# Kernel tuning notes

Hardware: AMD Instinct MI355X
Metric: run time of the kernel (lower is better)

The kernel has to match this reference:

```python
import jax, jax.numpy as jnp
import numpy as np

B, S, HID = 2, 2048, 3584
NH, NKV, HD = 16, 8, 256
WINDOW = 1024
SOFTCAP = 50.0


def setup_inputs() -> dict:
    key = jax.random.key(0)
    ks = jax.random.split(key, 8)
    hidden_states = jax.random.normal(ks[0], (B, S, HID), dtype=jnp.float32)
    attention_mask = jnp.ones((B, S), dtype=bool)
    position_ids = jnp.tile(jnp.arange(S, dtype=jnp.int32), (B, 1))
    # rotary tables indexed by position, last dim = head_dim
    inv_freq = 1.0 / (10000.0 ** (jnp.arange(0, HD, 2, dtype=jnp.float32) / HD))
    t = jnp.arange(S, dtype=jnp.float32)
    freqs = jnp.outer(t, inv_freq)  # [S, HD/2]
    emb = jnp.concatenate([freqs, freqs], axis=-1)  # [S, HD]
    sin, cos = jnp.sin(emb), jnp.cos(emb)
    causal_mask = jnp.tril(jnp.ones((1, 1, S, S), dtype=bool))
    sc = 0.02
    Wq = jax.random.normal(ks[1], (HID, NH * HD), dtype=jnp.float32) * sc
    Wk = jax.random.normal(ks[2], (HID, NKV * HD), dtype=jnp.float32) * sc
    Wv = jax.random.normal(ks[3], (HID, NKV * HD), dtype=jnp.float32) * sc
    Wo = jax.random.normal(ks[4], (NH * HD, HID), dtype=jnp.float32) * sc
    return {"hidden_states": hidden_states, "attention_mask": attention_mask,
            "position_ids": position_ids, "sin": sin, "cos": cos,
            "causal_mask": causal_mask, "Wq": Wq, "Wk": Wk, "Wv": Wv, "Wo": Wo}


def _rotate_half(x):
    x1, x2 = x[..., : x.shape[-1] // 2], x[..., x.shape[-1] // 2 :]
    return jnp.concatenate((-x2, x1), axis=-1)


def reference(hidden_states, attention_mask, position_ids, sin, cos, causal_mask, Wq, Wk, Wv, Wo):
    b, s, _ = hidden_states.shape
    q = (hidden_states @ Wq).reshape(b, s, NH, HD)
    k = (hidden_states @ Wk).reshape(b, s, NKV, HD)
    v = (hidden_states @ Wv).reshape(b, s, NKV, HD)

    # RoPE, applied in [b, h, s, d] layout as in the original
    s_ = sin[position_ids][:, None, :, :]  # [b,1,s,d]
    c_ = cos[position_ids][:, None, :, :]
    qh = q.transpose(0, 2, 1, 3)
    kh = k.transpose(0, 2, 1, 3)
    qh = qh * c_ + _rotate_half(qh) * s_
    kh = kh * c_ + _rotate_half(kh) * s_
    q = qh.transpose(0, 2, 1, 3)  # [b,s,nh,d]
    k = kh.transpose(0, 2, 1, 3)  # [b,s,nkv,d]

    # GQA: repeat kv heads to match query heads
    groups = NH // NKV
    k = jnp.repeat(k, groups, axis=2)  # [b,s,nh,d]
    v = jnp.repeat(v, groups, axis=2)

    # combine causal + padding masks, then sliding-window (even layer)
    mask = causal_mask[:, :, :s, :s] & attention_mask[:, None, None, :]  # [b,1,s,s]
    mask = jnp.broadcast_to(mask, (b, 1, s, s))
    far_past = jnp.tril(jnp.ones((s, s), dtype=bool), k=-WINDOW)[None, None]
    mask = mask & ~far_past

    neg = jnp.finfo(jnp.float32).min
    bias = jnp.where(mask, 0.0, neg).astype(jnp.float32)

    scale = HD ** -0.5
    logits = jnp.einsum("bqhd,bkhd->bhqk", q, k) * scale
    # Gemma2 logit softcapping
    logits = SOFTCAP * jnp.tanh(logits / SOFTCAP)
    logits = logits + bias
    probs = jax.nn.softmax(logits, axis=-1)
    out = jnp.einsum("bhqk,bkhd->bqhd", probs, v)
    out = out.reshape(b, s, NH * HD)
    return out @ Wo
```

## Files before the change

### kernel.cpp

```cpp
#include <hip/hip_runtime.h>
#include <hip/hip_bf16.h>

typedef __bf16 bf16x8_t __attribute__((ext_vector_type(8)));
typedef __bf16 bf16x4_t __attribute__((ext_vector_type(4)));
typedef short s16x4_t  __attribute__((ext_vector_type(4)));
typedef float f32x4_t  __attribute__((ext_vector_type(4)));

#define NB 2
#define NS 2048
#define NHID 3584
#define NHEADS 16
#define NKVH 8
#define DH 256
#define WIN 1024

__device__ __forceinline__ float bf2f(ushort u) {
  union { unsigned v; float f; } x; x.v = ((unsigned)u) << 16; return x.f;
}
__device__ __forceinline__ ushort f2bf(float f) {
  unsigned x = __builtin_bit_cast(unsigned, f);
  unsigned r = (x + 0x7fffu + ((x >> 16) & 1u)) >> 16;
  return (ushort)r;
}

__device__ __forceinline__ void gload16(const void* g, void* l) {
  __builtin_amdgcn_global_load_lds((const __attribute__((address_space(1))) void*)g,
                                   (__attribute__((address_space(3))) void*)l, 16, 0, 0);
}

__device__ __forceinline__ f32x4_t mfma_pv(s16x4_t a, s16x4_t b, f32x4_t c) {
#if __has_builtin(__builtin_amdgcn_mfma_f32_16x16x16_bf16)
  return __builtin_amdgcn_mfma_f32_16x16x16_bf16(
      __builtin_bit_cast(bf16x4_t, a), __builtin_bit_cast(bf16x4_t, b), c, 0, 0, 0);
#else
  return __builtin_amdgcn_mfma_f32_16x16x16bf16_1k(a, b, c, 0, 0, 0);
#endif
}

__device__ __forceinline__ float pexp(float s) {
  float e = __expf(fminf(s * 0.0025f, 80.f));
  float th = __fdividef(e - 1.f, e + 1.f);
  return __expf(50.f * th);
}

__global__ __launch_bounds__(256) void f32_to_bf16_kernel(const float* __restrict__ in,
                                                          ushort* __restrict__ out, int n4) {
  int i = (int)blockIdx.x * 256 + (int)threadIdx.x;
  if (i < n4) {
    float4 v = ((const float4*)in)[i];
    ushort4 o;
    o.x = f2bf(v.x); o.y = f2bf(v.y); o.z = f2bf(v.z); o.w = f2bf(v.w);
    ((ushort4*)out)[i] = o;
  }
}

__global__ __launch_bounds__(256) void transpose_f32_bf16(const float* __restrict__ in,
                                                          ushort* __restrict__ out,
                                                          int R, int Cc) {
  __shared__ ushort tile[64][72];
  const int t = threadIdx.x;
  const int ct = Cc >> 6;
  const int by = blockIdx.x / ct;
  const int bx = blockIdx.x % ct;
  const int r0 = by << 6, c0 = bx << 6;
#pragma unroll
  for (int i = 0; i < 16; ++i) {
    int idx = i * 256 + t;
    int r = idx >> 6, c = idx & 63;
    tile[r][c] = f2bf(in[(size_t)(r0 + r) * Cc + c0 + c]);
  }
  __syncthreads();
#pragma unroll
  for (int i = 0; i < 16; ++i) {
    int idx = i * 256 + t;
    int rr = idx >> 6, cc = idx & 63;
    out[(size_t)(c0 + rr) * R + r0 + cc] = tile[cc][rr];
  }
}

#define GSYNC1 do { __builtin_amdgcn_s_barrier(); \
    asm volatile("s_waitcnt lgkmcnt(0)" ::: "memory"); \
    __builtin_amdgcn_sched_barrier(0); } while (0)
#define GSYNC2(st) do { \
    if (st) asm volatile("s_waitcnt vmcnt(2)" ::: "memory"); \
    else    asm volatile("s_waitcnt vmcnt(0)" ::: "memory"); \
    __builtin_amdgcn_sched_barrier(0); \
    __builtin_amdgcn_s_barrier(); } while (0)

template <int EPI>
__global__ __launch_bounds__(512, 2) void gemm256(const ushort* __restrict__ A,
                                                  const ushort* __restrict__ Bt,
                                                  void* __restrict__ Cout,
                                                  int M, int N, int K) {
  __shared__ alignas(16) char lds[131072];
  const int t = threadIdx.x;
  const int lane = t & 63;
  const int wid = t >> 6;
  const int wm = wid >> 2;
  const int wn = wid & 3;
  const int g = lane >> 4;
  const int lr = lane & 15;
  const int lrow8 = lane >> 3;
  const int lp = (lane & 7) ^ lrow8;

  const int nbn = N >> 8;
  const int nwg = (int)gridDim.x;
  const int bid = (int)blockIdx.x;
  const int swz = (bid & 7) * (nwg >> 3) + (bid >> 3);
  const int bm = swz / nbn, bn = swz % nbn;
  const int m0 = bm << 8, n0 = bn << 8;

  f32x4_t acc[8][4] = {};
  const int T = K >> 6;

  auto stageA = [&](int q, int koff, int bufn) {
    int row = (q << 6) + (wid << 3) + lrow8;
    gload16(A + (size_t)(m0 + row) * K + koff + (lp << 3),
            lds + bufn * 32768 + (q << 13) + (wid << 10));
  };
  auto stageB = [&](int q, int koff, int bufn) {
    int row = (q << 6) + (wid << 3) + lrow8;
    gload16(Bt + (size_t)(n0 + row) * K + koff + (lp << 3),
            lds + 65536 + bufn * 32768 + (q << 13) + (wid << 10));
  };

#pragma unroll
  for (int q = 0; q < 4; ++q) { stageA(q, 0, 0); stageB(q, 0, 0); }
  asm volatile("s_waitcnt vmcnt(0)" ::: "memory");
  __builtin_amdgcn_s_barrier();

  for (int tt = 0; tt < T; ++tt) {
    const int bc = tt & 1;
    const int bnx = bc ^ 1;
    const bool st = (tt + 1 < T);
    const int kn = (tt + 1) << 6;
    const char* cA = lds + bc * 32768;
    const char* cB = lds + 65536 + bc * 32768;
    bf16x8_t af[4], bfv[4];

    auto ldA = [&](int i, int mh, int ks) {
      int row = (wm << 7) + (mh << 6) + (i << 4) + lr;
      af[i] = *(const bf16x8_t*)(cA + (row << 7) + (((ks << 6) + (g << 4)) ^ ((row & 7) << 4)));
    };
    auto ldB = [&](int j, int ks) {
      int row = (wn << 6) + (j << 4) + lr;
      bfv[j] = *(const bf16x8_t*)(cB + (row << 7) + (((ks << 6) + (g << 4)) ^ ((row & 7) << 4)));
    };

#pragma unroll
    for (int i = 0; i < 4; ++i) ldA(i, 0, 0);
#pragma unroll
    for (int j = 0; j < 4; ++j) ldB(j, 0);
    if (st) { stageA(0, kn, bnx); stageA(2, kn, bnx); }
    GSYNC1;
    __builtin_amdgcn_s_setprio(1);
#pragma unroll
    for (int i = 0; i < 4; ++i)
#pragma unroll
      for (int j = 0; j < 4; ++j)
        acc[i][j] = __builtin_amdgcn_mfma_f32_16x16x32_bf16(af[i], bfv[j], acc[i][j], 0, 0, 0);
    __builtin_amdgcn_s_setprio(0);
    GSYNC2(st);

#pragma unroll
    for (int i = 0; i < 4; ++i) ldA(i, 1, 0);
    if (st) { stageB(0, kn, bnx); stageB(1, kn, bnx); }
    GSYNC1;
    __builtin_amdgcn_s_setprio(1);
#pragma unroll
    for (int i = 0; i < 4; ++i)
#pragma unroll
      for (int j = 0; j < 4; ++j)
        acc[4 + i][j] = __builtin_amdgcn_mfma_f32_16x16x32_bf16(af[i], bfv[j], acc[4 + i][j], 0, 0, 0);
    __builtin_amdgcn_s_setprio(0);
    GSYNC2(st);

#pragma unroll
    for (int i = 0; i < 4; ++i) ldA(i, 0, 1);
#pragma unroll
    for (int j = 0; j < 4; ++j) ldB(j, 1);
    if (st) { stageB(2, kn, bnx); stageB(3, kn, bnx); }
    GSYNC1;
    __builtin_amdgcn_s_setprio(1);
#pragma unroll
    for (int i = 0; i < 4; ++i)
#pragma unroll
      for (int j = 0; j < 4; ++j)
        acc[i][j] = __builtin_amdgcn_mfma_f32_16x16x32_bf16(af[i], bfv[j], acc[i][j], 0, 0, 0);
    __builtin_amdgcn_s_setprio(0);
    GSYNC2(st);

#pragma unroll
    for (int i = 0; i < 4; ++i) ldA(i, 1, 1);
    if (st) { stageA(1, kn, bnx); stageA(3, kn, bnx); }
    GSYNC1;
    __builtin_amdgcn_s_setprio(1);
#pragma unroll
    for (int i = 0; i < 4; ++i)
#pragma unroll
      for (int j = 0; j < 4; ++j)
        acc[4 + i][j] = __builtin_amdgcn_mfma_f32_16x16x32_bf16(af[i], bfv[j], acc[4 + i][j], 0, 0, 0);
    __builtin_amdgcn_s_setprio(0);
    GSYNC2(st);
  }

  __syncthreads();
  const bool trstage = (EPI == 4) && (n0 >= 2048);
  if (trstage) {
#pragma unroll
    for (int i = 0; i < 8; ++i)
#pragma unroll
      for (int j = 0; j < 4; ++j) {
        int col = (wn << 6) + (j << 4) + lr;
#pragma unroll
        for (int r = 0; r < 4; ++r) {
          int row = (wm << 7) + (i << 4) + (g << 2) + r;
          *(ushort*)(lds + (col << 9) + ((row << 1) ^ ((col & 7) << 4))) = f2bf(acc[i][j][r]);
        }
      }
  } else {
#pragma unroll
    for (int i = 0; i < 8; ++i)
#pragma unroll
      for (int j = 0; j < 4; ++j) {
        int col = (wn << 6) + (j << 4) + lr;
#pragma unroll
        for (int r = 0; r < 4; ++r) {
          int row = (wm << 7) + (i << 4) + (g << 2) + r;
          *(ushort*)(lds + (row << 9) + ((col << 1) ^ ((row & 7) << 4))) = f2bf(acc[i][j][r]);
        }
      }
  }
  __syncthreads();

  if (EPI == 0) {
    ushort* C = (ushort*)Cout;
#pragma unroll
    for (int it = 0; it < 16; ++it) {
      int idx = it * 512 + t;
      int row = idx >> 5, ch = idx & 31;
      uint4 v = *(const uint4*)(lds + (row << 9) + ((ch << 4) ^ ((row & 7) << 4)));
      *(uint4*)(C + (size_t)(m0 + row) * N + n0 + (ch << 3)) = v;
    }
  } else if (EPI == 4) {
    ushort* C = (ushort*)Cout;
    if (n0 < 2048) {
#pragma unroll
      for (int it = 0; it < 16; ++it) {
        int idx = it * 512 + t;
        int row = idx >> 5, ch = idx & 31;
        uint4 v = *(const uint4*)(lds + (row << 9) + ((ch << 4) ^ ((row & 7) << 4)));
        *(uint4*)(C + (size_t)(m0 + row) * 2048 + n0 + (ch << 3)) = v;
      }
    } else {
      ushort* vC = C + (size_t)4096 * 2048;
      const int bb = m0 >> 11;
      const int ss = m0 & (NS - 1);
#pragma unroll
      for (int it = 0; it < 16; ++it) {
        int idx = it * 512 + t;
        int dc = idx >> 5, ch = idx & 31;
        uint4 v = *(const uint4*)(lds + (dc << 9) + ((ch << 4) ^ ((dc & 7) << 4)));
        int gc = (n0 - 2048) + dc;
        int kvh = gc >> 8, d = gc & 255;
        *(uint4*)(vC + ((size_t)((bb * NKVH + kvh) * DH + d)) * NS + ss + (ch << 3)) = v;
      }
    }
  } else {
    float* Cf = (float*)Cout;
#pragma unroll
    for (int it = 0; it < 32; ++it) {
      int idx = it * 512 + t;
      int row = idx >> 6, qd = idx & 63;
      ushort4 hv = *(const ushort4*)(lds + (row << 9) + ((qd << 3) ^ ((row & 7) << 4)));
      float4 fv;
      fv.x = bf2f(hv.x); fv.y = bf2f(hv.y); fv.z = bf2f(hv.z); fv.w = bf2f(hv.w);
      *(float4*)(Cf + (size_t)(m0 + row) * N + n0 + (qd << 2)) = fv;
    }
  }
}

__global__ __launch_bounds__(256) void rope_kernel(ushort* __restrict__ buf,
                                                   const float* __restrict__ sint,
                                                   const float* __restrict__ cost,
                                                   int nheads) {
  int idx = (int)blockIdx.x * 256 + (int)threadIdx.x;
  int d = idx & 127;
  int h = (idx >> 7) % nheads;
  int tok = idx / (nheads << 7);
  int pos = tok & (NS - 1);
  float c = cost[pos * DH + d];
  float s = sint[pos * DH + d];
  size_t base = (size_t)tok * ((size_t)nheads * DH) + h * DH + d;
  float x1 = bf2f(buf[base]);
  float x2 = bf2f(buf[base + 128]);
  buf[base] = f2bf(x1 * c - x2 * s);
  buf[base + 128] = f2bf(x2 * c + x1 * s);
}

__global__ __launch_bounds__(256) void attn_kernel(const ushort* __restrict__ q,
                                                   const ushort* __restrict__ k,
                                                   const ushort* __restrict__ vt,
                                                   ushort* __restrict__ ao) {
  __shared__ alignas(16) char lK[2][16384];
  __shared__ alignas(16) char lV[2][16384];
  const int bid = (int)blockIdx.x;
  const int qb = bid & 31;
  const int h = (bid >> 5) & 15;
  const int b = bid >> 9;
  const int kvh = h >> 1;
  const int qb0 = qb << 6;
  const int t = threadIdx.x;
  const int lane = t & 63;
  const int w = t >> 6;
  const int g = lane >> 4;
  const int lr = lane & 15;

  const int qrow = qb0 + (w << 4) + lr;
  bf16x8_t qf[8];
  const ushort* qbase = q + (size_t)(b * NS + qrow) * (NHEADS * DH) + h * DH;
#pragma unroll
  for (int ks = 0; ks < 8; ++ks)
    qf[ks] = *(const bf16x8_t*)(qbase + (ks << 5) + (g << 3));

  float l_r = 0.f;
  f32x4_t oacc[16] = {};

  const int qminw = qb0 + (w << 4);
  const int qmaxw = qminw + 15;
  int t_lo = qb0 - (WIN - 1);
  if (t_lo < 0) t_lo = 0;
  t_lo &= ~31;
  const int t_hi = qb0 + 63;

  const ushort* kgb = k + (size_t)(b * NS) * (NKVH * DH) + kvh * DH;
  const ushort* vgb = vt + (size_t)((b * NKVH + kvh) * DH) * NS;

  auto stage = [&](int kt, int bi) {
    char* dk = lK[bi];
    char* dv = lV[bi];
#pragma unroll
    for (int j = 0; j < 4; ++j) {
      int row = (w << 3) + (j << 1) + (lane >> 5);
      int ck = (lane & 31) ^ (row & 7);
      gload16(kgb + (size_t)(kt + row) * (NKVH * DH) + (ck << 3),
              dk + (((w << 3) + (j << 1)) << 9));
      int dl = (w << 6) + (j << 4) + (lane >> 2);
      int cv = (lane & 3) ^ ((dl >> 1) & 3);
      gload16(vgb + (size_t)dl * NS + kt + (cv << 3),
              dv + (((w << 2) + j) << 10));
    }
  };

  int cur = 0;
  stage(t_lo, 0);
  __syncthreads();

  for (int kt = t_lo; kt <= t_hi; kt += 32) {
    if (kt + 32 <= t_hi) stage(kt + 32, cur ^ 1);
    const char* lk = lK[cur];
    const char* lv = lV[cur];
#pragma unroll
    for (int sub = 0; sub < 2; ++sub) {
      const int key0 = kt + (sub << 4);
      if (key0 > qmaxw) continue;
      if (key0 + 15 < qminw - (WIN - 1)) continue;

      f32x4_t sacc = {};
      __builtin_amdgcn_s_setprio(1);
#pragma unroll
      for (int ks = 0; ks < 8; ++ks) {
        int row = (sub << 4) + lr;
        bf16x8_t kf = *(const bf16x8_t*)(lk + (((row << 9) + (ks << 6) + (g << 4)) ^ ((row & 7) << 4)));
        sacc = __builtin_amdgcn_mfma_f32_16x16x32_bf16(kf, qf[ks], sacc, 0, 0, 0);
      }
      __builtin_amdgcn_s_setprio(0);

      float pvv[4];
      const bool full = (key0 + 15 <= qminw) && (key0 >= qmaxw - (WIN - 1));
      if (full) {
#pragma unroll
        for (int r = 0; r < 4; ++r) { pvv[r] = pexp(sacc[r]); l_r += pvv[r]; }
      } else {
#pragma unroll
        for (int r = 0; r < 4; ++r) {
          int key = key0 + (g << 2) + r;
          bool ok = (key <= qrow) && (qrow - key < WIN);
          pvv[r] = ok ? pexp(sacc[r]) : 0.f;
          l_r += pvv[r];
        }
      }

      s16x4_t pa;
      pa[0] = (short)f2bf(pvv[0]);
      pa[1] = (short)f2bf(pvv[1]);
      pa[2] = (short)f2bf(pvv[2]);
      pa[3] = (short)f2bf(pvv[3]);

      const int kb2 = (sub << 5) + (g << 3);
      __builtin_amdgcn_s_setprio(1);
#pragma unroll
      for (int dt = 0; dt < 16; ++dt) {
        int d = (dt << 4) + lr;
        s16x4_t vf = *(const s16x4_t*)(lv + ((d << 6) + (kb2 ^ (((d >> 1) & 3) << 4))));
        oacc[dt] = mfma_pv(pa, vf, oacc[dt]);
      }
      __builtin_amdgcn_s_setprio(0);
    }
    __syncthreads();
    cur ^= 1;
  }

  l_r += __shfl_xor(l_r, 16);
  l_r += __shfl_xor(l_r, 32);
  float dn[4];
#pragma unroll
  for (int r = 0; r < 4; ++r)
    dn[r] = 1.0f / __shfl(l_r, (g << 2) + r);

  const int orow0 = b * NS + qb0 + (w << 4) + (g << 2);
#pragma unroll
  for (int dt = 0; dt < 16; ++dt) {
    int col = h * DH + (dt << 4) + lr;
#pragma unroll
    for (int r = 0; r < 4; ++r) {
      ao[(size_t)(orow0 + r) * (NHEADS * DH) + col] = f2bf(oacc[dt][r] * dn[r]);
    }
  }
}

extern "C" void kernel_launch(void* const* d_in, const int* in_sizes, int n_in,
                              void* d_out, int out_size, void* d_ws, size_t ws_size,
                              hipStream_t stream) {
  const float* hs   = (const float*)d_in[0];
  const float* sint = (const float*)d_in[3];
  const float* cost = (const float*)d_in[4];
  const float* Wq = (const float*)d_in[6];
  const float* Wk = (const float*)d_in[7];
  const float* Wv = (const float*)d_in[8];
  const float* Wo = (const float*)d_in[9];

  char* ws = (char*)d_ws;
  size_t off = 0;
  auto alloc = [&](size_t bytes) {
    char* p = ws + off;
    off += (bytes + 255) & ~(size_t)255;
    return p;
  };
  ushort* hsb   = (ushort*)alloc((size_t)4096 * 3584 * 2);
  ushort* wT    = (ushort*)alloc((size_t)4096 * 3584 * 2);
  ushort* qbuf  = (ushort*)alloc((size_t)4096 * 4096 * 2);
  ushort* kbuf  = (ushort*)alloc((size_t)4096 * 2048 * 2);
  ushort* vtbuf = (ushort*)alloc((size_t)4096 * 2048 * 2);
  ushort* aobuf = qbuf;
  if (off > ws_size) return;

  f32_to_bf16_kernel<<<(4096 * 3584 / 4) / 256, 256, 0, stream>>>(hs, hsb, 4096 * 3584 / 4);

  transpose_f32_bf16<<<(3584 / 64) * (2048 / 64), 256, 0, stream>>>(Wk, wT, 3584, 2048);
  transpose_f32_bf16<<<(3584 / 64) * (2048 / 64), 256, 0, stream>>>(Wv, wT + (size_t)2048 * 3584, 3584, 2048);
  gemm256<4><<<16 * 16, 512, 0, stream>>>(hsb, wT, kbuf, 4096, 4096, 3584);

  transpose_f32_bf16<<<(3584 / 64) * (4096 / 64), 256, 0, stream>>>(Wq, wT, 3584, 4096);
  gemm256<0><<<16 * 16, 512, 0, stream>>>(hsb, wT, qbuf, 4096, 4096, 3584);

  rope_kernel<<<(4096 * 16 * 128) / 256, 256, 0, stream>>>(qbuf, sint, cost, 16);
  rope_kernel<<<(4096 * 8 * 128) / 256, 256, 0, stream>>>(kbuf, sint, cost, 8);

  attn_kernel<<<NB * NHEADS * (NS / 64), 256, 0, stream>>>(qbuf, kbuf, vtbuf, aobuf);

  transpose_f32_bf16<<<(4096 / 64) * (3584 / 64), 256, 0, stream>>>(Wo, wT, 4096, 3584);
  gemm256<2><<<16 * 14, 512, 0, stream>>>(aobuf, wT, d_out, 4096, 3584, 4096);
}
```

Baseline: 604.2 us.

## Replace async double-buffered LDS staging with register-prefetched single buffer

The attention kernel now prefetches the next K/V tile into registers with plain global loads and writes it into a single LDS buffer after each compute step, replacing the double-buffered direct global-to-LDS loads. The V tile gets a new LDS layout so each PV fragment is one contiguous 8-byte read per lane instead of a swizzled address. This halves LDS use, which may let more blocks share a CU, and simplifies address math. The cost is extra registers for the staged data and an added barrier per iteration, since LDS writes now sit between compute steps.

```diff
diff --git a/kernel.cpp b/kernel.cpp
--- a/kernel.cpp
+++ b/kernel.cpp
@@ -302,8 +302,8 @@
                                                    const ushort* __restrict__ k,
                                                    const ushort* __restrict__ vt,
                                                    ushort* __restrict__ ao) {
-  __shared__ alignas(16) char lK[2][16384];
-  __shared__ alignas(16) char lV[2][16384];
+  __shared__ alignas(16) char lK[16384];
+  __shared__ alignas(16) char lV[16384];
   const int bid = (int)blockIdx.x;
   const int qb = bid & 31;
   const int h = (bid >> 5) & 15;
@@ -332,34 +332,46 @@
   if (t_lo < 0) t_lo = 0;
   t_lo &= ~31;
   const int t_hi = qb0 + 63;
+  const int nt = ((t_hi - t_lo) >> 5) + 1;
 
   const ushort* kgb = k + (size_t)(b * NS) * (NKVH * DH) + kvh * DH;
   const ushort* vgb = vt + (size_t)((b * NKVH + kvh) * DH) * NS;
 
-  auto stage = [&](int kt, int bi) {
-    char* dk = lK[bi];
-    char* dv = lV[bi];
+  const int krow = t >> 3;
+  const int kc16 = (t & 7) << 2;
+  uint4 kr[4], vr[4];
+
+  auto ldreg = [&](int kt) {
+    const ushort* ks = kgb + (size_t)(kt + krow) * (NKVH * DH) + (kc16 << 3);
+#pragma unroll
+    for (int j = 0; j < 4; ++j) kr[j] = *(const uint4*)(ks + (j << 3));
+    const ushort* vs = vgb + (size_t)t * NS + kt;
+#pragma unroll
+    for (int j = 0; j < 4; ++j) vr[j] = *(const uint4*)(vs + (j << 3));
+  };
+  auto wlds = [&]() {
 #pragma unroll
     for (int j = 0; j < 4; ++j) {
-      int row = (w << 3) + (j << 1) + (lane >> 5);
-      int ck = (lane & 31) ^ (row & 7);
-      gload16(kgb + (size_t)(kt + row) * (NKVH * DH) + (ck << 3),
-              dk + (((w << 3) + (j << 1)) << 9));
-      int dl = (w << 6) + (j << 4) + (lane >> 2);
-      int cv = (lane & 3) ^ ((dl >> 1) & 3);
-      gload16(vgb + (size_t)dl * NS + kt + (cv << 3),
-              dv + (((w << 2) + j) << 10));
+      int pc = (kc16 + j) ^ (krow & 7);
+      *(uint4*)(lK + (krow << 9) + (pc << 4)) = kr[j];
+    }
+    char* vb = lV + ((t >> 4) << 10) + ((t & 15) << 3);
+#pragma unroll
+    for (int j = 0; j < 4; ++j) {
+      uint2 lo; lo.x = vr[j].x; lo.y = vr[j].y;
+      uint2 hi; hi.x = vr[j].z; hi.y = vr[j].w;
+      *(uint2*)(vb + ((j << 1) << 7)) = lo;
+      *(uint2*)(vb + (((j << 1) | 1) << 7)) = hi;
     }
   };
 
-  int cur = 0;
-  stage(t_lo, 0);
+  ldreg(t_lo);
+  wlds();
+  if (nt > 1) ldreg(t_lo + 32);
   __syncthreads();
 
-  for (int kt = t_lo; kt <= t_hi; kt += 32) {
-    if (kt + 32 <= t_hi) stage(kt + 32, cur ^ 1);
-    const char* lk = lK[cur];
-    const char* lv = lV[cur];
+  for (int i = 0; i < nt; ++i) {
+    const int kt = t_lo + (i << 5);
 #pragma unroll
     for (int sub = 0; sub < 2; ++sub) {
       const int key0 = kt + (sub << 4);
@@ -371,7 +383,7 @@
 #pragma unroll
       for (int ks = 0; ks < 8; ++ks) {
         int row = (sub << 4) + lr;
-        bf16x8_t kf = *(const bf16x8_t*)(lk + (((row << 9) + (ks << 6) + (g << 4)) ^ ((row & 7) << 4)));
+        bf16x8_t kf = *(const bf16x8_t*)(lK + (((row << 9) + (ks << 6) + (g << 4)) ^ ((row & 7) << 4)));
         sacc = __builtin_amdgcn_mfma_f32_16x16x32_bf16(kf, qf[ks], sacc, 0, 0, 0);
       }
       __builtin_amdgcn_s_setprio(0);
@@ -397,18 +409,21 @@
       pa[2] = (short)f2bf(pvv[2]);
       pa[3] = (short)f2bf(pvv[3]);
 
-      const int kb2 = (sub << 5) + (g << 3);
+      const int vsub = ((sub << 2) + g) << 7;
       __builtin_amdgcn_s_setprio(1);
 #pragma unroll
       for (int dt = 0; dt < 16; ++dt) {
-        int d = (dt << 4) + lr;
-        s16x4_t vf = *(const s16x4_t*)(lv + ((d << 6) + (kb2 ^ (((d >> 1) & 3) << 4))));
+        s16x4_t vf = *(const s16x4_t*)(lV + (dt << 10) + vsub + (lr << 3));
         oacc[dt] = mfma_pv(pa, vf, oacc[dt]);
       }
       __builtin_amdgcn_s_setprio(0);
     }
     __syncthreads();
-    cur ^= 1;
+    if (i + 1 < nt) {
+      wlds();
+      if (i + 2 < nt) ldreg(t_lo + ((i + 2) << 5));
+      __syncthreads();
+    }
   }
 
   l_r += __shfl_xor(l_r, 16);
```

After: 708.4 us. +17.2%, slower.

## Pre-tile V in MFMA fragment order and widen attention blocks to 128 queries

Applied to the files above, without the earlier changes.

The K/V GEMM epilogue now writes V in a pre-tiled layout: 32-key blocks of 8192 elements arranged in the exact order the PV MFMA fragment reads expect. Attention staging therefore becomes a contiguous 16-byte copy and the LDS reads for V need no swizzle math. The attention kernel also moves to 512 threads covering 128 query rows per block, so each K/V tile loaded into LDS is reused by twice as many query rows. The costs are fewer blocks in the grid (512 instead of 1024), more masked-out work inside the wider causal and window range, and a V layout that only this kernel understands.

```diff
diff --git a/kernel.cpp b/kernel.cpp
--- a/kernel.cpp
+++ b/kernel.cpp
@@ -254,16 +254,18 @@
       }
     } else {
       ushort* vC = C + (size_t)4096 * 2048;
-      const int bb = m0 >> 11;
-      const int ss = m0 & (NS - 1);
+      const int plane = (m0 >> 11) * NKVH + ((n0 - 2048) >> 8);
+      ushort* dst = vC + (size_t)plane * ((size_t)NS * DH) + (size_t)((m0 & (NS - 1)) >> 5) * 8192;
 #pragma unroll
       for (int it = 0; it < 16; ++it) {
-        int idx = it * 512 + t;
-        int dc = idx >> 5, ch = idx & 31;
-        uint4 v = *(const uint4*)(lds + (dc << 9) + ((ch << 4) ^ ((dc & 7) << 4)));
-        int gc = (n0 - 2048) + dc;
-        int kvh = gc >> 8, d = gc & 255;
-        *(uint4*)(vC + ((size_t)((bb * NKVH + kvh) * DH + d)) * NS + ss + (ch << 3)) = v;
+        int s = it * 512 + t;
+        int lr2 = s & 7, kq = (s >> 3) & 7, dt_l = (s >> 6) & 15, sb_l = s >> 10;
+        int d0 = (dt_l << 4) + (lr2 << 1);
+        int r0 = (sb_l << 5) + (kq << 2);
+        uint2 a = *(const uint2*)(lds + (d0 << 9) + ((r0 << 1) ^ ((d0 & 7) << 4)));
+        uint2 b2 = *(const uint2*)(lds + ((d0 + 1) << 9) + ((r0 << 1) ^ (((d0 + 1) & 7) << 4)));
+        uint4 v; v.x = a.x; v.y = a.y; v.z = b2.x; v.w = b2.y;
+        *(uint4*)(dst + (size_t)s * 8) = v;
       }
     }
   } else {
@@ -298,18 +300,18 @@
   buf[base + 128] = f2bf(x2 * c + x1 * s);
 }
 
-__global__ __launch_bounds__(256) void attn_kernel(const ushort* __restrict__ q,
+__global__ __launch_bounds__(512) void attn_kernel(const ushort* __restrict__ q,
                                                    const ushort* __restrict__ k,
                                                    const ushort* __restrict__ vt,
                                                    ushort* __restrict__ ao) {
   __shared__ alignas(16) char lK[2][16384];
   __shared__ alignas(16) char lV[2][16384];
   const int bid = (int)blockIdx.x;
-  const int qb = bid & 31;
-  const int h = (bid >> 5) & 15;
-  const int b = bid >> 9;
+  const int qb = bid & 15;
+  const int h = (bid >> 4) & 15;
+  const int b = bid >> 8;
   const int kvh = h >> 1;
-  const int qb0 = qb << 6;
+  const int qb0 = qb << 7;
   const int t = threadIdx.x;
   const int lane = t & 63;
   const int w = t >> 6;
@@ -331,24 +333,23 @@
   int t_lo = qb0 - (WIN - 1);
   if (t_lo < 0) t_lo = 0;
   t_lo &= ~31;
-  const int t_hi = qb0 + 63;
+  const int t_hi = qb0 + 127;
+  const int nt = ((t_hi - t_lo) >> 5) + 1;
 
   const ushort* kgb = k + (size_t)(b * NS) * (NKVH * DH) + kvh * DH;
-  const ushort* vgb = vt + (size_t)((b * NKVH + kvh) * DH) * NS;
+  const ushort* vgb = vt + (size_t)(b * NKVH + kvh) * ((size_t)NS * DH);
 
   auto stage = [&](int kt, int bi) {
     char* dk = lK[bi];
     char* dv = lV[bi];
-#pragma unroll
-    for (int j = 0; j < 4; ++j) {
-      int row = (w << 3) + (j << 1) + (lane >> 5);
+    const int sb = kt >> 5;
+#pragma unroll
+    for (int j = 0; j < 2; ++j) {
+      int i = (w << 1) + j;
+      int row = (i << 1) + (lane >> 5);
       int ck = (lane & 31) ^ (row & 7);
-      gload16(kgb + (size_t)(kt + row) * (NKVH * DH) + (ck << 3),
-              dk + (((w << 3) + (j << 1)) << 9));
-      int dl = (w << 6) + (j << 4) + (lane >> 2);
-      int cv = (lane & 3) ^ ((dl >> 1) & 3);
-      gload16(vgb + (size_t)dl * NS + kt + (cv << 3),
-              dv + (((w << 2) + j) << 10));
+      gload16(kgb + (size_t)(kt + row) * (NKVH * DH) + (ck << 3), dk + (i << 10));
+      gload16(vgb + (size_t)sb * 8192 + (((i << 6) + lane) << 3), dv + (i << 10));
     }
   };
 
@@ -356,8 +357,9 @@
   stage(t_lo, 0);
   __syncthreads();
 
-  for (int kt = t_lo; kt <= t_hi; kt += 32) {
-    if (kt + 32 <= t_hi) stage(kt + 32, cur ^ 1);
+  for (int i = 0; i < nt; ++i) {
+    const int kt = t_lo + (i << 5);
+    if (i + 1 < nt) stage(kt + 32, cur ^ 1);
     const char* lk = lK[cur];
     const char* lv = lV[cur];
 #pragma unroll
@@ -397,12 +399,11 @@
       pa[2] = (short)f2bf(pvv[2]);
       pa[3] = (short)f2bf(pvv[3]);
 
-      const int kb2 = (sub << 5) + (g << 3);
+      const int kqoff = ((sub << 2) + g) << 7;
       __builtin_amdgcn_s_setprio(1);
 #pragma unroll
       for (int dt = 0; dt < 16; ++dt) {
-        int d = (dt << 4) + lr;
-        s16x4_t vf = *(const s16x4_t*)(lv + ((d << 6) + (kb2 ^ (((d >> 1) & 3) << 4))));
+        s16x4_t vf = *(const s16x4_t*)(lv + (dt << 10) + kqoff + (lr << 3));
         oacc[dt] = mfma_pv(pa, vf, oacc[dt]);
       }
       __builtin_amdgcn_s_setprio(0);
@@ -467,7 +468,7 @@
   rope_kernel<<<(4096 * 16 * 128) / 256, 256, 0, stream>>>(qbuf, sint, cost, 16);
   rope_kernel<<<(4096 * 8 * 128) / 256, 256, 0, stream>>>(kbuf, sint, cost, 8);
 
-  attn_kernel<<<NB * NHEADS * (NS / 64), 256, 0, stream>>>(qbuf, kbuf, vtbuf, aobuf);
+  attn_kernel<<<NB * NHEADS * (NS / 128), 512, 0, stream>>>(qbuf, kbuf, vtbuf, aobuf);
 
   transpose_f32_bf16<<<(4096 / 64) * (3584 / 64), 256, 0, stream>>>(Wo, wT, 4096, 3584);
   gemm256<2><<<16 * 14, 512, 0, stream>>>(aobuf, wT, d_out, 4096, 3584, 4096);
```

Measured after the change: 603.1 us. No clear change (-0.2%).
